# Kernel optimization log

Measured on AMD Instinct MI355X. Metric: run time of the kernel, lower is better.

The kernel has to match this reference:

```python
import jax, jax.numpy as jnp
import numpy as np

B = 16384
D_MODEL = 1024
HIDDEN = 2048  # 2 * d_model (expansion_factor=2)
G0_IN = 512    # concatenated group [t0, t1]
REST_IN = 256  # six remaining single-term groups
N_REST = 6
SEQ_LEN = 7
EPS = 1e-05
W_SCALE = 0.02  # keep SwiGLU activations numerically tame


def setup_inputs() -> dict:
    key = jax.random.key(0)
    ks = jax.random.split(key, 8)
    return {
        "obs": jax.random.normal(ks[0], (B, 2048), dtype=jnp.float32),
        "w1_g0": jax.random.normal(ks[1], (HIDDEN, G0_IN), dtype=jnp.float32) * W_SCALE,
        "w3_g0": jax.random.normal(ks[2], (HIDDEN, G0_IN), dtype=jnp.float32) * W_SCALE,
        "w2_g0": jax.random.normal(ks[3], (D_MODEL, HIDDEN), dtype=jnp.float32) * W_SCALE,
        "w1_r": jax.random.normal(ks[4], (N_REST, HIDDEN, REST_IN), dtype=jnp.float32) * W_SCALE,
        "w3_r": jax.random.normal(ks[5], (N_REST, HIDDEN, REST_IN), dtype=jnp.float32) * W_SCALE,
        "w2_r": jax.random.normal(ks[6], (N_REST, D_MODEL, HIDDEN), dtype=jnp.float32) * W_SCALE,
        "norm_w": jnp.ones((D_MODEL,), dtype=jnp.float32),
        "norm_b": jnp.zeros((D_MODEL,), dtype=jnp.float32),
        "term_embed": jax.random.normal(ks[7], (SEQ_LEN, D_MODEL), dtype=jnp.float32),
    }


def reference(obs, w1_g0, w3_g0, w2_g0, w1_r, w3_r, w2_r, norm_w, norm_b, term_embed):
    # Group 0: concat of terms t0,t1 -> obs[:, :512]
    x0 = obs[:, :G0_IN]                                   # [B, 512]
    gate0 = jax.nn.silu(x0 @ w1_g0.T)                     # [B, H]
    tok0 = (gate0 * (x0 @ w3_g0.T)) @ w2_g0.T             # [B, D]

    # Remaining 6 single-term groups of width 256, batched as one einsum
    xr = obs[:, G0_IN:].reshape(B, N_REST, REST_IN)       # [B, G, 256]
    gate = jax.nn.silu(jnp.einsum('bgi,ghi->bgh', xr, w1_r))
    val = jnp.einsum('bgi,ghi->bgh', xr, w3_r)
    tok_r = jnp.einsum('bgh,gdh->bgd', gate * val, w2_r)  # [B, G, D]

    x = jnp.concatenate([tok0[:, None, :], tok_r], axis=1)  # [B, 7, D]

    # RMSNorm (no mean subtraction), computed in fp32
    xf = x.astype(jnp.float32)
    rms = jnp.sqrt(jnp.mean(xf * xf, axis=-1, keepdims=True) + EPS)
    x = ((xf / rms) * norm_w + norm_b).astype(x.dtype)

    # learned term (position) embedding, broadcast over batch
    return x + term_embed[None, :, :]
```

## Files before the change

kernel.cpp:

```cpp
#include <hip/hip_runtime.h>

typedef _Float16 f16;
typedef _Float16 f16x8 __attribute__((ext_vector_type(8)));
typedef _Float16 f16x4 __attribute__((ext_vector_type(4)));
typedef float f32x4 __attribute__((ext_vector_type(4)));

#define MFMA_F16(A, B, C) __builtin_amdgcn_mfma_f32_16x16x32_f16(A, B, C, 0, 0, 0)

#define TM 128
#define TN 128
#define BK 64
#define LSTR 80

__device__ __forceinline__ void stage_tile(const f16* __restrict__ g, int ldg,
                                           f16* __restrict__ s) {
    const int t = threadIdx.x;
#pragma unroll
    for (int i = 0; i < 4; ++i) {
        int c = i * 256 + t;
        int row = c >> 3, p = c & 7;
        uint4 v = *(const uint4*)(g + (size_t)row * ldg + p * 8);
        *(uint4*)(s + row * LSTR + p * 8) = v;
    }
}

__global__ __launch_bounds__(256) void k1_gate(
    const f16* __restrict__ A, int K,
    const f16* __restrict__ W1, const f16* __restrict__ W3,
    f16* __restrict__ Hout)
{
    __shared__ f16 smem[3 * TM * LSTR];
    f16* As  = smem;
    f16* B1s = smem + TM * LSTR;
    f16* B3s = smem + 2 * TM * LSTR;

    const int hb = blockIdx.x;
    const int rb = blockIdx.y;
    const int wave = threadIdx.x >> 6;
    const int lane = threadIdx.x & 63;
    const int wr = wave >> 1, wc = wave & 1;
    const int ln = lane & 15, lq = lane >> 4;

    f32x4 acc1[4][4] = {};
    f32x4 acc3[4][4] = {};

    const f16* Ab  = A  + (size_t)rb * TM * 2048;
    const f16* B1b = W1 + (size_t)hb * TN * K;
    const f16* B3b = W3 + (size_t)hb * TN * K;

    for (int k0 = 0; k0 < K; k0 += BK) {
        __syncthreads();
        stage_tile(Ab + k0, 2048, As);
        stage_tile(B1b + k0, K, B1s);
        stage_tile(B3b + k0, K, B3s);
        __syncthreads();
#pragma unroll
        for (int ks = 0; ks < 2; ++ks) {
            f16x8 af[4], b1f[4], b3f[4];
#pragma unroll
            for (int mi = 0; mi < 4; ++mi)
                af[mi] = *(const f16x8*)(As + (wr * 64 + mi * 16 + ln) * LSTR + ks * 32 + lq * 8);
#pragma unroll
            for (int ni = 0; ni < 4; ++ni) {
                b1f[ni] = *(const f16x8*)(B1s + (wc * 64 + ni * 16 + ln) * LSTR + ks * 32 + lq * 8);
                b3f[ni] = *(const f16x8*)(B3s + (wc * 64 + ni * 16 + ln) * LSTR + ks * 32 + lq * 8);
            }
#pragma unroll
            for (int mi = 0; mi < 4; ++mi)
#pragma unroll
                for (int ni = 0; ni < 4; ++ni) {
                    acc1[mi][ni] = MFMA_F16(af[mi], b1f[ni], acc1[mi][ni]);
                    acc3[mi][ni] = MFMA_F16(af[mi], b3f[ni], acc3[mi][ni]);
                }
        }
    }

    __syncthreads();
    const int CT = 136;
    f16* Ct = smem;
#pragma unroll
    for (int mi = 0; mi < 4; ++mi)
#pragma unroll
        for (int r = 0; r < 4; ++r) {
            int lrow = wr * 64 + mi * 16 + lq * 4 + r;
#pragma unroll
            for (int ni = 0; ni < 4; ++ni) {
                float g1 = acc1[mi][ni][r];
                float g3 = acc3[mi][ni][r];
                float h = g1 / (1.f + __expf(-g1)) * g3;
                Ct[lrow * CT + wc * 64 + ni * 16 + ln] = (f16)h;
            }
        }
    __syncthreads();
    const size_t row0g = (size_t)rb * TM;
    const int col0g = hb * TN;
    const int t = threadIdx.x;
#pragma unroll
    for (int i = 0; i < 8; ++i) {
        int c = i * 256 + t;
        int row = c >> 4, p = c & 15;
        *(uint4*)(Hout + (row0g + row) * 2048 + col0g + p * 8) =
            *(const uint4*)(Ct + row * CT + p * 8);
    }
}

#define K2NT 32
__global__ __launch_bounds__(512, 2) void k2_out(
    const f16* __restrict__ Hm, const f16* __restrict__ W2,
    float* __restrict__ outp,
    float* __restrict__ ssp)
{
    __shared__ f16 As[2][256 * 64];
    __shared__ f16 Bs[2][256 * 64];
    __shared__ float ssTile[256];

    const int bid = blockIdx.x;
    const int swz = (bid & 7) * 32 + (bid >> 3);
    const int cb = swz & 3;
    const int rb = swz >> 2;

    const int wid = threadIdx.x >> 6;
    const int lane = threadIdx.x & 63;
    const int wm = wid >> 2;
    const int wn = wid & 3;
    const int ln = lane & 15, lq = lane >> 4;

    if (threadIdx.x < 256) ssTile[threadIdx.x] = 0.f;

    const f16* Ab = Hm + (size_t)rb * 256 * 2048;
    const f16* Bb = W2 + (size_t)cb * 256 * 2048;

#define K2_STAGE(kt, b)                                                                     \
    {                                                                                       \
        const f16* ga = Ab + (kt) * 64;                                                     \
        const f16* gb = Bb + (kt) * 64;                                                     \
        const int tt = threadIdx.x;                                                         \
        _Pragma("unroll")                                                                   \
        for (int i = 0; i < 4; ++i) {                                                       \
            int c = i * 512 + tt;                                                           \
            int row = c >> 3, p = c & 7, ps = p ^ (row & 7);                                \
            __builtin_amdgcn_global_load_lds(                                               \
                (const __attribute__((address_space(1))) void*)(ga + (size_t)row * 2048 + ps * 8), \
                (__attribute__((address_space(3))) void*)(&As[b][c * 8]), 16, 0, 0);        \
        }                                                                                   \
        _Pragma("unroll")                                                                   \
        for (int i = 0; i < 4; ++i) {                                                       \
            int c = i * 512 + tt;                                                           \
            int row = c >> 3, p = c & 7, ps = p ^ (row & 7);                                \
            __builtin_amdgcn_global_load_lds(                                               \
                (const __attribute__((address_space(1))) void*)(gb + (size_t)row * 2048 + ps * 8), \
                (__attribute__((address_space(3))) void*)(&Bs[b][c * 8]), 16, 0, 0);        \
        }                                                                                   \
    }

    K2_STAGE(0, 0);
    K2_STAGE(1, 1);

    f32x4 acc[8][4] = {};

    for (int t = 0; t < K2NT; ++t) {
        const int b = t & 1;
        asm volatile("s_waitcnt vmcnt(8)" ::: "memory");
        __builtin_amdgcn_sched_barrier(0);
        __builtin_amdgcn_s_barrier();

        const char* Ap = (const char*)&As[b][0];
        const char* Bp = (const char*)&Bs[b][0];

        f16x8 bf[4][2], af[4][2];
#pragma unroll
        for (int ni = 0; ni < 4; ++ni)
#pragma unroll
            for (int ks = 0; ks < 2; ++ks) {
                int row = wn * 64 + ni * 16 + ln;
                bf[ni][ks] = *(const f16x8*)(Bp + row * 128 + ((ks * 64 + lq * 16) ^ ((row & 7) << 4)));
            }
#pragma unroll
        for (int mi = 0; mi < 4; ++mi)
#pragma unroll
            for (int ks = 0; ks < 2; ++ks) {
                int row = wm * 128 + mi * 16 + ln;
                af[mi][ks] = *(const f16x8*)(Ap + row * 128 + ((ks * 64 + lq * 16) ^ ((row & 7) << 4)));
            }
        asm volatile("s_waitcnt lgkmcnt(0)" ::: "memory");
        __builtin_amdgcn_sched_barrier(0);

        __builtin_amdgcn_s_setprio(1);
#pragma unroll
        for (int mi = 0; mi < 4; ++mi)
#pragma unroll
            for (int ni = 0; ni < 4; ++ni) {
                acc[mi][ni] = MFMA_F16(af[mi][0], bf[ni][0], acc[mi][ni]);
                acc[mi][ni] = MFMA_F16(af[mi][1], bf[ni][1], acc[mi][ni]);
            }
        __builtin_amdgcn_s_setprio(0);

#pragma unroll
        for (int mi = 0; mi < 4; ++mi)
#pragma unroll
            for (int ks = 0; ks < 2; ++ks) {
                int row = wm * 128 + 64 + mi * 16 + ln;
                af[mi][ks] = *(const f16x8*)(Ap + row * 128 + ((ks * 64 + lq * 16) ^ ((row & 7) << 4)));
            }
        asm volatile("s_waitcnt lgkmcnt(0)" ::: "memory");
        __builtin_amdgcn_sched_barrier(0);
        __builtin_amdgcn_s_barrier();

        K2_STAGE((t + 2) & (K2NT - 1), b);

        __builtin_amdgcn_s_setprio(1);
#pragma unroll
        for (int mi = 0; mi < 4; ++mi)
#pragma unroll
            for (int ni = 0; ni < 4; ++ni) {
                acc[4 + mi][ni] = MFMA_F16(af[mi][0], bf[ni][0], acc[4 + mi][ni]);
                acc[4 + mi][ni] = MFMA_F16(af[mi][1], bf[ni][1], acc[4 + mi][ni]);
            }
        __builtin_amdgcn_s_setprio(0);
    }

    const size_t grow0 = (size_t)rb * 256 + wm * 128;
    const int gcol0 = cb * 256 + wn * 64;
#pragma unroll
    for (int mi8 = 0; mi8 < 8; ++mi8)
#pragma unroll
        for (int r = 0; r < 4; ++r) {
            int lrl = (mi8 >> 2) * 64 + (mi8 & 3) * 16 + lq * 4 + r;
            int lrow = wm * 128 + lrl;
            size_t grow = grow0 + lrl;
            float s = 0.f;
#pragma unroll
            for (int ni = 0; ni < 4; ++ni) {
                float c = acc[mi8][ni][r];
                s += c * c;
                outp[grow * 7168 + gcol0 + ni * 16 + ln] = c;
            }
            s += __shfl_xor(s, 1);
            s += __shfl_xor(s, 2);
            s += __shfl_xor(s, 4);
            s += __shfl_xor(s, 8);
            if (ln == 0) atomicAdd(&ssTile[lrow], s);
        }
    __syncthreads();
    if (threadIdx.x < 256)
        ssp[(size_t)cb * 16384 + rb * 256 + threadIdx.x] = ssTile[threadIdx.x];
}

__global__ __launch_bounds__(256) void k3_norm(
    float* __restrict__ outp, const float* __restrict__ ss,
    const float* __restrict__ nw, const float* __restrict__ nb,
    const float* __restrict__ te)
{
    const int rrow = blockIdx.x;
    const int g = rrow % 7;
    const int b = rrow / 7;
    float ssum = 0.f;
#pragma unroll
    for (int cb = 0; cb < 4; ++cb) ssum += ss[(size_t)(g * 4 + cb) * 16384 + b];
    const float rinv = 1.0f / sqrtf(ssum * (1.0f / 1024.0f) + 1e-5f);
    const int t = threadIdx.x;
    float4* rowp = (float4*)(outp + (size_t)rrow * 1024);
    float4 x = rowp[t];
    float4 w = ((const float4*)nw)[t];
    float4 bb = ((const float4*)nb)[t];
    float4 e = ((const float4*)(te + g * 1024))[t];
    float4 o;
    o.x = x.x * rinv * w.x + bb.x + e.x;
    o.y = x.y * rinv * w.y + bb.y + e.y;
    o.z = x.z * rinv * w.z + bb.z + e.z;
    o.w = x.w * rinv * w.w + bb.w + e.w;
    rowp[t] = o;
}

__global__ __launch_bounds__(256) void cvt_f16(const float* __restrict__ s, f16* __restrict__ d) {
    size_t i = (size_t)blockIdx.x * 256 + threadIdx.x;
    float4 v = ((const float4*)s)[i];
    f16x4 o = { (f16)v.x, (f16)v.y, (f16)v.z, (f16)v.w };
    ((f16x4*)d)[i] = o;
}

extern "C" void kernel_launch(void* const* d_in, const int* in_sizes, int n_in,
                              void* d_out, int out_size, void* d_ws, size_t ws_size,
                              hipStream_t stream) {
    const float* obs  = (const float*)d_in[0];
    const float* w1g0 = (const float*)d_in[1];
    const float* w3g0 = (const float*)d_in[2];
    const float* w2g0 = (const float*)d_in[3];
    const float* w1r  = (const float*)d_in[4];
    const float* w3r  = (const float*)d_in[5];
    const float* w2r  = (const float*)d_in[6];
    const float* nw   = (const float*)d_in[7];
    const float* nb   = (const float*)d_in[8];
    const float* te   = (const float*)d_in[9];

    f16* obs_h  = (f16*)d_ws;
    f16* w1g0_h = obs_h  + 33554432;
    f16* w3g0_h = w1g0_h + 1048576;
    f16* w2g0_h = w3g0_h + 1048576;
    f16* w1r_h  = w2g0_h + 2097152;
    f16* w3r_h  = w1r_h  + 3145728;
    f16* w2r_h  = w3r_h  + 3145728;
    f16* Hbuf   = w2r_h  + 12582912;
    float* ssb  = (float*)(Hbuf + 33554432);

    cvt_f16<<<33554432 / 1024, 256, 0, stream>>>(obs, obs_h);
    cvt_f16<<<1048576 / 1024, 256, 0, stream>>>(w1g0, w1g0_h);
    cvt_f16<<<1048576 / 1024, 256, 0, stream>>>(w3g0, w3g0_h);
    cvt_f16<<<2097152 / 1024, 256, 0, stream>>>(w2g0, w2g0_h);
    cvt_f16<<<3145728 / 1024, 256, 0, stream>>>(w1r, w1r_h);
    cvt_f16<<<3145728 / 1024, 256, 0, stream>>>(w3r, w3r_h);
    cvt_f16<<<12582912 / 1024, 256, 0, stream>>>(w2r, w2r_h);

    for (int g = 0; g < 7; ++g) {
        const f16* A  = obs_h + (g == 0 ? 0 : 512 + (g - 1) * 256);
        int K         = (g == 0) ? 512 : 256;
        const f16* W1 = (g == 0) ? w1g0_h : w1r_h + (size_t)(g - 1) * 2048 * 256;
        const f16* W3 = (g == 0) ? w3g0_h : w3r_h + (size_t)(g - 1) * 2048 * 256;
        const f16* W2 = (g == 0) ? w2g0_h : w2r_h + (size_t)(g - 1) * 1024 * 2048;
        k1_gate<<<dim3(16, 128), 256, 0, stream>>>(A, K, W1, W3, Hbuf);
        k2_out<<<256, 512, 0, stream>>>(Hbuf, W2, (float*)d_out + g * 1024,
                                        ssb + (size_t)g * 4 * 16384);
    }
    k3_norm<<<114688, 256, 0, stream>>>((float*)d_out, ssb, nw, nb, te);
}
```

Measured before the change: 1.941 ms.

## Rewrite gate GEMM with double-buffered async LDS loads, swizzle, larger tiles

```diff
diff --git a/kernel.cpp b/kernel.cpp
--- a/kernel.cpp
+++ b/kernel.cpp
@@ -7,101 +7,150 @@
 
 #define MFMA_F16(A, B, C) __builtin_amdgcn_mfma_f32_16x16x32_f16(A, B, C, 0, 0, 0)
 
-#define TM 128
-#define TN 128
-#define BK 64
-#define LSTR 80
-
-__device__ __forceinline__ void stage_tile(const f16* __restrict__ g, int ldg,
-                                           f16* __restrict__ s) {
-    const int t = threadIdx.x;
-#pragma unroll
-    for (int i = 0; i < 4; ++i) {
-        int c = i * 256 + t;
-        int row = c >> 3, p = c & 7;
-        uint4 v = *(const uint4*)(g + (size_t)row * ldg + p * 8);
-        *(uint4*)(s + row * LSTR + p * 8) = v;
-    }
-}
-
-__global__ __launch_bounds__(256) void k1_gate(
+__global__ __launch_bounds__(512, 2) void k1_gate(
     const f16* __restrict__ A, int K,
     const f16* __restrict__ W1, const f16* __restrict__ W3,
     f16* __restrict__ Hout)
 {
-    __shared__ f16 smem[3 * TM * LSTR];
-    f16* As  = smem;
-    f16* B1s = smem + TM * LSTR;
-    f16* B3s = smem + 2 * TM * LSTR;
-
-    const int hb = blockIdx.x;
-    const int rb = blockIdx.y;
-    const int wave = threadIdx.x >> 6;
+    __shared__ f16 As[2][256 * 64];
+    __shared__ f16 B1s[2][128 * 64];
+    __shared__ f16 B3s[2][128 * 64];
+
+    const int bid = blockIdx.x;
+    const int swz = (bid & 7) * 128 + (bid >> 3);
+    const int hb = swz & 15;
+    const int rb = swz >> 4;
+
+    const int wid = threadIdx.x >> 6;
     const int lane = threadIdx.x & 63;
-    const int wr = wave >> 1, wc = wave & 1;
+    const int wm = wid >> 1;
+    const int wn = wid & 1;
     const int ln = lane & 15, lq = lane >> 4;
+
+    const f16* Ab  = A  + (size_t)rb * 256 * 2048;
+    const f16* B1b = W1 + (size_t)hb * 128 * K;
+    const f16* B3b = W3 + (size_t)hb * 128 * K;
+    const int NT = K >> 6;
+
+#define K1_STAGE(kt, b)                                                                     \
+    {                                                                                       \
+        const f16* ga = Ab + (kt) * 64;                                                     \
+        const f16* g1 = B1b + (kt) * 64;                                                    \
+        const f16* g3 = B3b + (kt) * 64;                                                    \
+        const int tt = threadIdx.x;                                                         \
+        _Pragma("unroll")                                                                   \
+        for (int i = 0; i < 4; ++i) {                                                       \
+            int c = i * 512 + tt;                                                           \
+            int row = c >> 3, p = c & 7, ps = p ^ (row & 7);                                \
+            __builtin_amdgcn_global_load_lds(                                               \
+                (const __attribute__((address_space(1))) void*)(ga + (size_t)row * 2048 + ps * 8), \
+                (__attribute__((address_space(3))) void*)(&As[b][c * 8]), 16, 0, 0);        \
+        }                                                                                   \
+        _Pragma("unroll")                                                                   \
+        for (int i = 0; i < 2; ++i) {                                                       \
+            int c = i * 512 + tt;                                                           \
+            int row = c >> 3, p = c & 7, ps = p ^ (row & 7);                                \
+            __builtin_amdgcn_global_load_lds(                                               \
+                (const __attribute__((address_space(1))) void*)(g1 + (size_t)row * K + ps * 8), \
+                (__attribute__((address_space(3))) void*)(&B1s[b][c * 8]), 16, 0, 0);       \
+        }                                                                                   \
+        _Pragma("unroll")                                                                   \
+        for (int i = 0; i < 2; ++i) {                                                       \
+            int c = i * 512 + tt;                                                           \
+            int row = c >> 3, p = c & 7, ps = p ^ (row & 7);                                \
+            __builtin_amdgcn_global_load_lds(                                               \
+                (const __attribute__((address_space(1))) void*)(g3 + (size_t)row * K + ps * 8), \
+                (__attribute__((address_space(3))) void*)(&B3s[b][c * 8]), 16, 0, 0);       \
+        }                                                                                   \
+    }
+
+    K1_STAGE(0, 0);
+    K1_STAGE(1, 1);
 
     f32x4 acc1[4][4] = {};
     f32x4 acc3[4][4] = {};
 
-    const f16* Ab  = A  + (size_t)rb * TM * 2048;
-    const f16* B1b = W1 + (size_t)hb * TN * K;
-    const f16* B3b = W3 + (size_t)hb * TN * K;
-
-    for (int k0 = 0; k0 < K; k0 += BK) {
-        __syncthreads();
-        stage_tile(Ab + k0, 2048, As);
-        stage_tile(B1b + k0, K, B1s);
-        stage_tile(B3b + k0, K, B3s);
-        __syncthreads();
-#pragma unroll
-        for (int ks = 0; ks < 2; ++ks) {
-            f16x8 af[4], b1f[4], b3f[4];
-#pragma unroll
-            for (int mi = 0; mi < 4; ++mi)
-                af[mi] = *(const f16x8*)(As + (wr * 64 + mi * 16 + ln) * LSTR + ks * 32 + lq * 8);
-#pragma unroll
-            for (int ni = 0; ni < 4; ++ni) {
-                b1f[ni] = *(const f16x8*)(B1s + (wc * 64 + ni * 16 + ln) * LSTR + ks * 32 + lq * 8);
-                b3f[ni] = *(const f16x8*)(B3s + (wc * 64 + ni * 16 + ln) * LSTR + ks * 32 + lq * 8);
-            }
-#pragma unroll
-            for (int mi = 0; mi < 4; ++mi)
-#pragma unroll
-                for (int ni = 0; ni < 4; ++ni) {
-                    acc1[mi][ni] = MFMA_F16(af[mi], b1f[ni], acc1[mi][ni]);
-                    acc3[mi][ni] = MFMA_F16(af[mi], b3f[ni], acc3[mi][ni]);
-                }
+    for (int t = 0; t < NT; ++t) {
+        const int b = t & 1;
+        if (t < NT - 1) {
+            asm volatile("s_waitcnt vmcnt(8)" ::: "memory");
+        } else {
+            asm volatile("s_waitcnt vmcnt(0)" ::: "memory");
         }
-    }
-
-    __syncthreads();
-    const int CT = 136;
-    f16* Ct = smem;
+        __builtin_amdgcn_sched_barrier(0);
+        __builtin_amdgcn_s_barrier();
+
+        const char* Ap = (const char*)&As[b][0];
+        const char* Bp1 = (const char*)&B1s[b][0];
+        const char* Bp3 = (const char*)&B3s[b][0];
+
+        f16x8 af[4][2], bf[4][2];
+#pragma unroll
+        for (int mi = 0; mi < 4; ++mi)
+#pragma unroll
+            for (int ks = 0; ks < 2; ++ks) {
+                int row = wm * 64 + mi * 16 + ln;
+                af[mi][ks] = *(const f16x8*)(Ap + row * 128 + ((ks * 64 + lq * 16) ^ ((row & 7) << 4)));
+            }
+#pragma unroll
+        for (int ni = 0; ni < 4; ++ni)
+#pragma unroll
+            for (int ks = 0; ks < 2; ++ks) {
+                int row = wn * 64 + ni * 16 + ln;
+                bf[ni][ks] = *(const f16x8*)(Bp1 + row * 128 + ((ks * 64 + lq * 16) ^ ((row & 7) << 4)));
+            }
+        asm volatile("s_waitcnt lgkmcnt(0)" ::: "memory");
+        __builtin_amdgcn_sched_barrier(0);
+
+        __builtin_amdgcn_s_setprio(1);
+#pragma unroll
+        for (int mi = 0; mi < 4; ++mi)
+#pragma unroll
+            for (int ni = 0; ni < 4; ++ni) {
+                acc1[mi][ni] = MFMA_F16(af[mi][0], bf[ni][0], acc1[mi][ni]);
+                acc1[mi][ni] = MFMA_F16(af[mi][1], bf[ni][1], acc1[mi][ni]);
+            }
+        __builtin_amdgcn_s_setprio(0);
+
+#pragma unroll
+        for (int ni = 0; ni < 4; ++ni)
+#pragma unroll
+            for (int ks = 0; ks < 2; ++ks) {
+                int row = wn * 64 + ni * 16 + ln;
+                bf[ni][ks] = *(const f16x8*)(Bp3 + row * 128 + ((ks * 64 + lq * 16) ^ ((row & 7) << 4)));
+            }
+        asm volatile("s_waitcnt lgkmcnt(0)" ::: "memory");
+        __builtin_amdgcn_sched_barrier(0);
+        __builtin_amdgcn_s_barrier();
+
+        if (t + 2 < NT) K1_STAGE(t + 2, b);
+
+        __builtin_amdgcn_s_setprio(1);
+#pragma unroll
+        for (int mi = 0; mi < 4; ++mi)
+#pragma unroll
+            for (int ni = 0; ni < 4; ++ni) {
+                acc3[mi][ni] = MFMA_F16(af[mi][0], bf[ni][0], acc3[mi][ni]);
+                acc3[mi][ni] = MFMA_F16(af[mi][1], bf[ni][1], acc3[mi][ni]);
+            }
+        __builtin_amdgcn_s_setprio(0);
+    }
+
+    const size_t row0 = (size_t)rb * 256 + wm * 64;
+    const int col0 = hb * 128 + wn * 64;
 #pragma unroll
     for (int mi = 0; mi < 4; ++mi)
 #pragma unroll
         for (int r = 0; r < 4; ++r) {
-            int lrow = wr * 64 + mi * 16 + lq * 4 + r;
+            size_t row = row0 + mi * 16 + lq * 4 + r;
 #pragma unroll
             for (int ni = 0; ni < 4; ++ni) {
                 float g1 = acc1[mi][ni][r];
                 float g3 = acc3[mi][ni][r];
                 float h = g1 / (1.f + __expf(-g1)) * g3;
-                Ct[lrow * CT + wc * 64 + ni * 16 + ln] = (f16)h;
+                Hout[row * 2048 + col0 + ni * 16 + ln] = (f16)h;
             }
         }
-    __syncthreads();
-    const size_t row0g = (size_t)rb * TM;
-    const int col0g = hb * TN;
-    const int t = threadIdx.x;
-#pragma unroll
-    for (int i = 0; i < 8; ++i) {
-        int c = i * 256 + t;
-        int row = c >> 4, p = c & 15;
-        *(uint4*)(Hout + (row0g + row) * 2048 + col0g + p * 8) =
-            *(const uint4*)(Ct + row * CT + p * 8);
-    }
 }
 
 #define K2NT 32
@@ -317,7 +366,7 @@
         const f16* W1 = (g == 0) ? w1g0_h : w1r_h + (size_t)(g - 1) * 2048 * 256;
         const f16* W3 = (g == 0) ? w3g0_h : w3r_h + (size_t)(g - 1) * 2048 * 256;
         const f16* W2 = (g == 0) ? w2g0_h : w2r_h + (size_t)(g - 1) * 1024 * 2048;
-        k1_gate<<<dim3(16, 128), 256, 0, stream>>>(A, K, W1, W3, Hbuf);
+        k1_gate<<<1024, 512, 0, stream>>>(A, K, W1, W3, Hbuf);
         k2_out<<<256, 512, 0, stream>>>(Hbuf, W2, (float*)d_out + g * 1024,
                                         ssb + (size_t)g * 4 * 16384);
     }
```

Result: faster. 1.703 ms (-12.3%).
